# Optimization experiments

Hardware: AMD Instinct MI355X
Metric: run time of the kernel (lower is better)

The kernel has to match this reference:

```python
import jax, jax.numpy as jnp
import numpy as np

D_MODEL = 256
NUM_HEADS = 4
D_K = D_MODEL // NUM_HEADS
SCALE = float(np.sqrt(D_K))


def setup_inputs() -> dict:
    key = jax.random.key(0)
    ks = jax.random.split(key, 11)
    B, S, D = 8, 2048, D_MODEL
    inp = {
        "query": jax.random.normal(ks[0], (B, S, D), dtype=jnp.float32),
        "key": jax.random.normal(ks[1], (B, S, D), dtype=jnp.float32),
        "value": jax.random.normal(ks[2], (B, S, D), dtype=jnp.float32),
        "W_q": jax.random.normal(ks[3], (D, D), dtype=jnp.float32) / np.sqrt(D),
        "b_q": jnp.zeros((D,), dtype=jnp.float32),
        "W_k": jax.random.normal(ks[4], (D, D), dtype=jnp.float32) / np.sqrt(D),
        "b_k": jnp.zeros((D,), dtype=jnp.float32),
        "W_v": jax.random.normal(ks[5], (D, D), dtype=jnp.float32) / np.sqrt(D),
        "b_v": jnp.zeros((D,), dtype=jnp.float32),
        "W_o": jax.random.normal(ks[6], (D, D), dtype=jnp.float32) / np.sqrt(D),
        "b_o": jnp.zeros((D,), dtype=jnp.float32),
    }
    return inp


def reference(query, key, value, W_q, b_q, W_k, b_k, W_v, b_v, W_o, b_o):
    B, Sq, D = query.shape
    Sk = key.shape[1]
    H, dk = NUM_HEADS, D_K
    # projections (torch Linear equivalent: x @ W + b with W as (in,out))
    Q = (query @ W_q + b_q).reshape(B, Sq, H, dk).transpose(0, 2, 1, 3)  # (B,H,Sq,dk)
    K = (key @ W_k + b_k).reshape(B, Sk, H, dk).transpose(0, 2, 1, 3)    # (B,H,Sk,dk)
    V = value @ W_v + b_v                                                # (B,Sk,D) shared across heads
    scores = jnp.einsum("bhqd,bhkd->bhqk", Q, K) / SCALE                 # (B,H,Sq,Sk)
    attn = jax.nn.softmax(scores, axis=-1)
    avg_attn = attn.mean(axis=1)                                         # (B,Sq,Sk)
    out = jnp.einsum("bqk,bkd->bqd", avg_attn, V)
    out = out @ W_o + b_o
    return out, avg_attn
```

## Files before the change

### kernel.cpp

```cpp
#include <hip/hip_runtime.h>
#include <stdint.h>

#define S2048 2048
#define DMODEL 256
#define NH 4
#define DK 64

typedef __bf16 bf16x8 __attribute__((ext_vector_type(8)));
typedef float f32x4 __attribute__((ext_vector_type(4)));

#define MFMA16(a, b, c) __builtin_amdgcn_mfma_f32_16x16x32_bf16((a), (b), (c), 0, 0, 0)

__device__ __forceinline__ uint16_t f2bf(float f) {
  uint32_t u = __builtin_bit_cast(uint32_t, f);
  u = (u + 0x7fff + ((u >> 16) & 1)) >> 16;
  return (uint16_t)u;
}

__device__ __forceinline__ void async16(const void* g, void* l) {
  __builtin_amdgcn_global_load_lds(
      (const __attribute__((address_space(1))) unsigned int*)g,
      (__attribute__((address_space(3))) unsigned int*)l, 16, 0, 0);
}

__device__ __forceinline__ void stage64(const char* gbase, int rstride,
                                        char* lds, int tid, int rows) {
  int iters = rows >> 5;
#pragma unroll
  for (int it = 0; it < iters; ++it) {
    int cid = (it << 8) + tid;
    int m = cid >> 3, cp = cid & 7, c = cp ^ (m & 7);
    async16(gbase + (size_t)m * rstride + (c << 4),
            lds + ((size_t)((it << 8) + (tid & ~63)) << 4));
  }
}

__device__ __forceinline__ bf16x8 frag_ld(const char* t, int rowbase, int chunk, int l15) {
  int m = rowbase + l15;
  return *(const bf16x8*)(t + (((m << 3) + (chunk ^ (m & 7))) << 4));
}

__device__ __forceinline__ bf16x8 frag_ld32(const char* t, int rowbase, int chunk, int l15) {
  int m = rowbase + l15;
  return *(const bf16x8*)(t + (((m << 2) + (chunk ^ (m & 3))) << 4));
}

__global__ __launch_bounds__(256) void cast_x(const float* __restrict__ q,
                                              const float* __restrict__ k,
                                              const float* __restrict__ v,
                                              uint16_t* __restrict__ xq,
                                              uint16_t* __restrict__ xk,
                                              uint16_t* __restrict__ xv) {
  const float* src = blockIdx.y == 0 ? q : (blockIdx.y == 1 ? k : v);
  uint16_t* dst = blockIdx.y == 0 ? xq : (blockIdx.y == 1 ? xk : xv);
  size_t i = ((size_t)blockIdx.x * 256 + threadIdx.x) * 8;
  float4 a = *(const float4*)(src + i);
  float4 b = *(const float4*)(src + i + 4);
  union { uint16_t s[8]; uint4 u; } r;
  r.s[0] = f2bf(a.x); r.s[1] = f2bf(a.y); r.s[2] = f2bf(a.z); r.s[3] = f2bf(a.w);
  r.s[4] = f2bf(b.x); r.s[5] = f2bf(b.y); r.s[6] = f2bf(b.z); r.s[7] = f2bf(b.w);
  *(uint4*)(dst + i) = r.u;
}

__global__ __launch_bounds__(256) void cast_w(const float* __restrict__ Wq,
                                              const float* __restrict__ Wk,
                                              const float* __restrict__ Wv,
                                              const float* __restrict__ Wo,
                                              uint16_t* __restrict__ Wqt,
                                              uint16_t* __restrict__ Wkt,
                                              uint16_t* __restrict__ Wvt,
                                              uint16_t* __restrict__ Wot) {
  const float* W = blockIdx.y == 0 ? Wq : blockIdx.y == 1 ? Wk : blockIdx.y == 2 ? Wv : Wo;
  uint16_t* Wt = blockIdx.y == 0 ? Wqt : blockIdx.y == 1 ? Wkt : blockIdx.y == 2 ? Wvt : Wot;
  __shared__ uint16_t t[64 * 66];
  int tile = blockIdx.x, tr = tile >> 2, tc = tile & 3;
  int tid = threadIdx.x;
#pragma unroll
  for (int i = 0; i < 16; ++i) {
    int e = i * 256 + tid, r = e >> 6, cl = e & 63;
    t[r * 66 + cl] = f2bf(W[(size_t)(tr * 64 + r) * 256 + tc * 64 + cl]);
  }
  __syncthreads();
#pragma unroll
  for (int i = 0; i < 16; ++i) {
    int e = i * 256 + tid, n = e >> 6, kk = e & 63;
    Wt[(size_t)(tc * 64 + n) * 256 + tr * 64 + kk] = t[kk * 66 + n];
  }
}

template <int OUTF32, int BIAS>
__global__ __launch_bounds__(256) void gemm_bt(const uint16_t* __restrict__ A,
                                               const uint16_t* __restrict__ Bt,
                                               const float* __restrict__ bias,
                                               void* __restrict__ Cv, int K, int ldc) {
  __shared__ char lds[32768];
  char* At = lds;
  char* Btl = lds + 16384;
  int tid = threadIdx.x, lane = tid & 63, wid = tid >> 6;
  int l15 = lane & 15, q = lane >> 4;
  int mt = blockIdx.x, nt = blockIdx.y;
  int wm = (wid >> 1) * 64, wn = (wid & 1) * 64;
  f32x4 acc[4][4] = {};
  const char* Ag = (const char*)(A + (size_t)(mt * 128) * K);
  const char* Bg = (const char*)(Bt + (size_t)(nt * 128) * K);
  int nk = K >> 6;
  for (int kt = 0; kt < nk; ++kt) {
    stage64(Ag + kt * 128, K * 2, At, tid, 128);
    stage64(Bg + kt * 128, K * 2, Btl, tid, 128);
    __syncthreads();
#pragma unroll
    for (int ks = 0; ks < 2; ++ks) {
      bf16x8 a[4], b[4];
#pragma unroll
      for (int i = 0; i < 4; ++i) a[i] = frag_ld(At, wm + i * 16, ks * 4 + q, l15);
#pragma unroll
      for (int j = 0; j < 4; ++j) b[j] = frag_ld(Btl, wn + j * 16, ks * 4 + q, l15);
#pragma unroll
      for (int i = 0; i < 4; ++i)
#pragma unroll
        for (int j = 0; j < 4; ++j) acc[i][j] = MFMA16(a[i], b[j], acc[i][j]);
    }
    __syncthreads();
  }
#pragma unroll
  for (int i = 0; i < 4; ++i) {
    int r0 = mt * 128 + wm + i * 16 + q * 4;
#pragma unroll
    for (int j = 0; j < 4; ++j) {
      int c = nt * 128 + wn + j * 16 + l15;
#pragma unroll
      for (int e = 0; e < 4; ++e) {
        float v = acc[i][j][e];
        if (BIAS == 1) v += bias[c];
        if (BIAS == 2) v += bias[r0 + e];
        size_t off = (size_t)(r0 + e) * ldc + c;
        if (OUTF32) ((float*)Cv)[off] = v;
        else ((uint16_t*)Cv)[off] = f2bf(v);
      }
    }
  }
}

__global__ __launch_bounds__(256) void attn_lsum(const uint16_t* __restrict__ Qb,
                                                 const uint16_t* __restrict__ Kb,
                                                 float* __restrict__ linv4) {
  __shared__ char lds[32768];
  char* Qt = lds;
  char* Kt = lds + 16384;
  int tid = threadIdx.x, lane = tid & 63, wid = tid >> 6;
  int l15 = lane & 15, q = lane >> 4;
  int b = blockIdx.z, h = blockIdx.y, qt = blockIdx.x;
  const char* Qg = (const char*)(Qb + ((size_t)b * S2048 + qt * 128) * DMODEL + h * DK);
  const char* Kg = (const char*)(Kb + ((size_t)b * S2048) * DMODEL + h * DK);
  stage64(Qg, DMODEL * 2, Qt, tid, 128);
  float ps[2][4] = {};
  for (int kt = 0; kt < 16; ++kt) {
    stage64(Kg + (size_t)kt * 128 * (DMODEL * 2), DMODEL * 2, Kt, tid, 128);
    __syncthreads();
#pragma unroll
    for (int i = 0; i < 2; ++i) {
      bf16x8 a0 = frag_ld(Qt, wid * 32 + i * 16, q, l15);
      bf16x8 a1 = frag_ld(Qt, wid * 32 + i * 16, 4 + q, l15);
#pragma unroll
      for (int j = 0; j < 8; ++j) {
        f32x4 s = {0.f, 0.f, 0.f, 0.f};
        s = MFMA16(a0, frag_ld(Kt, j * 16, q, l15), s);
        s = MFMA16(a1, frag_ld(Kt, j * 16, 4 + q, l15), s);
#pragma unroll
        for (int e = 0; e < 4; ++e) ps[i][e] += __expf(s[e] * 0.125f);
      }
    }
    __syncthreads();
  }
#pragma unroll
  for (int i = 0; i < 2; ++i)
#pragma unroll
    for (int e = 0; e < 4; ++e) {
      float v = ps[i][e];
      v += __shfl_xor(v, 1); v += __shfl_xor(v, 2);
      v += __shfl_xor(v, 4); v += __shfl_xor(v, 8);
      if (l15 == 0) {
        int row = qt * 128 + wid * 32 + i * 16 + q * 4 + e;
        linv4[((size_t)(b * NH + h)) * S2048 + row] = 0.25f / v;
      }
    }
}

__global__ __launch_bounds__(256) void attn_fused(const uint16_t* __restrict__ Qb,
                                                  const uint16_t* __restrict__ Kb,
                                                  const uint16_t* __restrict__ VbT,
                                                  const float* __restrict__ linv4,
                                                  float* __restrict__ attn,
                                                  uint16_t* __restrict__ out1) {
  __shared__ __align__(16) char lds[51200];
  char* Kt = lds;
  char* Vt = lds + 16384;
  char* Pt = lds + 49152;
  int tid = threadIdx.x, lane = tid & 63, wid = tid >> 6;
  int l15 = lane & 15, hi = lane >> 4;
  int b = blockIdx.x & 7, qt = blockIdx.x >> 3;
  int qbase = qt * 32;
  int wq = wid & 1, wk = wid >> 1;
  int qg = wid & 1, dg = wid >> 1;
  const char* Qg = (const char*)(Qb + ((size_t)b * S2048 + qbase) * DMODEL);
  const char* Kg = (const char*)(Kb + (size_t)b * S2048 * DMODEL);
  const char* Vgb = (const char*)(VbT + (size_t)b * S2048);
#pragma unroll
  for (int h = 0; h < NH; ++h)
    stage64(Qg + h * 128, DMODEL * 2, Kt + h * 4096, tid, 32);
  float li[NH][4];
#pragma unroll
  for (int h = 0; h < NH; ++h)
#pragma unroll
    for (int e = 0; e < 4; ++e)
      li[h][e] = linv4[((size_t)(b * NH + h)) * S2048 + qbase + wq * 16 + hi * 4 + e];
  __syncthreads();
  bf16x8 qf[NH][2];
#pragma unroll
  for (int h = 0; h < NH; ++h)
#pragma unroll
    for (int ks = 0; ks < 2; ++ks)
      qf[h][ks] = frag_ld(Kt + h * 4096, wq * 16, ks * 4 + hi, l15);
  __syncthreads();
#pragma unroll
  for (int h = 0; h < NH; ++h)
    stage64(Kg + h * 128, DMODEL * 2, Kt + h * 4096, tid, 32);
  stage64(Vgb, 32768, Vt, tid, 256);
  __syncthreads();
  f32x4 acc[8] = {};
  size_t arow0 = (size_t)b * S2048 + qbase + wq * 16 + hi * 4;
#pragma unroll 2
  for (int kt = 0; kt < 64; ++kt) {
    float Pav[4] = {0.f, 0.f, 0.f, 0.f};
#pragma unroll
    for (int h = 0; h < NH; ++h) {
      f32x4 s = {0.f, 0.f, 0.f, 0.f};
      s = MFMA16(qf[h][0], frag_ld(Kt + h * 4096, wk * 16, hi, l15), s);
      s = MFMA16(qf[h][1], frag_ld(Kt + h * 4096, wk * 16, 4 + hi, l15), s);
#pragma unroll
      for (int e = 0; e < 4; ++e) Pav[e] += __expf(s[e] * 0.125f) * li[h][e];
    }
#pragma unroll
    for (int e = 0; e < 4; ++e) {
      int m = wq * 16 + hi * 4 + e, kk = wk * 16 + l15;
      *(uint16_t*)(Pt + (((m << 2) + ((kk >> 3) ^ (m & 3))) << 4) + ((kk & 7) << 1)) =
          f2bf(Pav[e]);
    }
    __syncthreads();
    {
      int kc = kt * 32 + wk * 16 + l15;
#pragma unroll
      for (int e = 0; e < 4; ++e) attn[(arow0 + e) * S2048 + kc] = Pav[e];
    }
    if (kt + 1 < 64) {
#pragma unroll
      for (int h = 0; h < NH; ++h)
        stage64(Kg + (size_t)(kt + 1) * 32 * (DMODEL * 2) + h * 128, DMODEL * 2,
                Kt + h * 4096, tid, 32);
    }
    {
      int ks = kt & 1;
      bf16x8 pa = frag_ld32(Pt, qg * 16, hi, l15);
#pragma unroll
      for (int j = 0; j < 8; ++j) {
        bf16x8 vb = frag_ld(Vt, dg * 128 + j * 16, ks * 4 + hi, l15);
        acc[j] = MFMA16(pa, vb, acc[j]);
      }
    }
    __syncthreads();
    if ((kt & 1) && kt + 1 < 64)
      stage64(Vgb + (size_t)((kt + 1) >> 1) * 128, 32768, Vt, tid, 256);
  }
#pragma unroll
  for (int j = 0; j < 8; ++j) {
    size_t r0 = (size_t)b * S2048 + qbase + qg * 16 + hi * 4;
    int c = dg * 128 + j * 16 + l15;
#pragma unroll
    for (int e = 0; e < 4; ++e) out1[(r0 + e) * DMODEL + c] = f2bf(acc[j][e]);
  }
}

extern "C" void kernel_launch(void* const* d_in, const int* in_sizes, int n_in,
                              void* d_out, int out_size, void* d_ws, size_t ws_size,
                              hipStream_t stream) {
  const float* query = (const float*)d_in[0];
  const float* key_i = (const float*)d_in[1];
  const float* value = (const float*)d_in[2];
  const float* W_q = (const float*)d_in[3];
  const float* b_q = (const float*)d_in[4];
  const float* W_k = (const float*)d_in[5];
  const float* b_k = (const float*)d_in[6];
  const float* W_v = (const float*)d_in[7];
  const float* b_v = (const float*)d_in[8];
  const float* W_o = (const float*)d_in[9];
  const float* b_o = (const float*)d_in[10];

  char* ws = (char*)d_ws;
  const size_t SZX = 16384ull * 256 * 2;
  uint16_t* Xq = (uint16_t*)(ws + 0 * SZX);
  uint16_t* Xk = (uint16_t*)(ws + 1 * SZX);
  uint16_t* Xv = (uint16_t*)(ws + 2 * SZX);
  uint16_t* Qb = (uint16_t*)(ws + 3 * SZX);
  uint16_t* Kb = (uint16_t*)(ws + 4 * SZX);
  uint16_t* VbT = (uint16_t*)(ws + 5 * SZX);
  uint16_t* out1b = (uint16_t*)(ws + 6 * SZX);
  uint16_t* Wqt = (uint16_t*)(ws + 7 * SZX);
  uint16_t* Wkt = (uint16_t*)(ws + 7 * SZX + 131072);
  uint16_t* Wvt = (uint16_t*)(ws + 7 * SZX + 2 * 131072);
  uint16_t* Wot = (uint16_t*)(ws + 7 * SZX + 3 * 131072);
  float* linv4 = (float*)(ws + 7 * SZX + 4 * 131072);

  float* out = (float*)d_out;
  float* attn = out + 16384ull * 256;

  cast_x<<<dim3(2048, 3), 256, 0, stream>>>(query, key_i, value, Xq, Xk, Xv);
  cast_w<<<dim3(16, 4), 256, 0, stream>>>(W_q, W_k, W_v, W_o, Wqt, Wkt, Wvt, Wot);
  gemm_bt<0, 1><<<dim3(128, 2), 256, 0, stream>>>(Xq, Wqt, b_q, Qb, 256, 256);
  gemm_bt<0, 1><<<dim3(128, 2), 256, 0, stream>>>(Xk, Wkt, b_k, Kb, 256, 256);
  gemm_bt<0, 2><<<dim3(2, 128), 256, 0, stream>>>(Wvt, Xv, b_v, VbT, 256, 16384);
  attn_lsum<<<dim3(16, 4, 8), 256, 0, stream>>>(Qb, Kb, linv4);
  attn_fused<<<dim3(512), 256, 0, stream>>>(Qb, Kb, VbT, linv4, attn, out1b);
  gemm_bt<1, 1><<<dim3(128, 2), 256, 0, stream>>>(out1b, Wot, b_o, out, 256, 256);
}
```

Measured before the change: 343.4 us.

## Restructure attention kernels: 512-thread fused tile, direct V loads, double-buffered lsum

Folds the 1/sqrt(dk) scale into the Q projection epilogue so the attention kernels drop a multiply before each exp. attn_lsum now hoists Q fragments into registers and double-buffers K tiles in LDS so the next tile loads while the current one computes. attn_fused moves to 512 threads with 64-key tiles, halving loop iterations and barriers, and reads V fragments straight from global memory into registers rather than staging V through LDS. This frees LDS and may improve occupancy, but adds per-lane global V loads and doubles register pressure per block, and rounding the scaled Q to bf16 slightly changes numerics.

```diff
diff --git a/kernel.cpp b/kernel.cpp
--- a/kernel.cpp
+++ b/kernel.cpp
@@ -35,14 +35,21 @@
   }
 }
 
+__device__ __forceinline__ void stage64b(const char* gbase, int rstride,
+                                         char* lds, int tid, int rows) {
+  int iters = rows >> 6;
+#pragma unroll
+  for (int it = 0; it < iters; ++it) {
+    int cid = (it << 9) + tid;
+    int m = cid >> 3, cp = cid & 7, c = cp ^ (m & 7);
+    async16(gbase + (size_t)m * rstride + (c << 4),
+            lds + ((size_t)((it << 9) + (tid & ~63)) << 4));
+  }
+}
+
 __device__ __forceinline__ bf16x8 frag_ld(const char* t, int rowbase, int chunk, int l15) {
   int m = rowbase + l15;
   return *(const bf16x8*)(t + (((m << 3) + (chunk ^ (m & 7))) << 4));
-}
-
-__device__ __forceinline__ bf16x8 frag_ld32(const char* t, int rowbase, int chunk, int l15) {
-  int m = rowbase + l15;
-  return *(const bf16x8*)(t + (((m << 2) + (chunk ^ (m & 3))) << 4));
 }
 
 __global__ __launch_bounds__(256) void cast_x(const float* __restrict__ q,
@@ -92,7 +99,8 @@
 __global__ __launch_bounds__(256) void gemm_bt(const uint16_t* __restrict__ A,
                                                const uint16_t* __restrict__ Bt,
                                                const float* __restrict__ bias,
-                                               void* __restrict__ Cv, int K, int ldc) {
+                                               void* __restrict__ Cv, int K, int ldc,
+                                               float scale) {
   __shared__ char lds[32768];
   char* At = lds;
   char* Btl = lds + 16384;
@@ -133,6 +141,7 @@
         float v = acc[i][j][e];
         if (BIAS == 1) v += bias[c];
         if (BIAS == 2) v += bias[r0 + e];
+        v *= scale;
         size_t off = (size_t)(r0 + e) * ldc + c;
         if (OUTF32) ((float*)Cv)[off] = v;
         else ((uint16_t*)Cv)[off] = f2bf(v);
@@ -144,30 +153,42 @@
 __global__ __launch_bounds__(256) void attn_lsum(const uint16_t* __restrict__ Qb,
                                                  const uint16_t* __restrict__ Kb,
                                                  float* __restrict__ linv4) {
-  __shared__ char lds[32768];
+  __shared__ char lds[49152];
   char* Qt = lds;
-  char* Kt = lds + 16384;
+  char* Kt0 = lds + 16384;
+  char* Kt1 = lds + 32768;
   int tid = threadIdx.x, lane = tid & 63, wid = tid >> 6;
   int l15 = lane & 15, q = lane >> 4;
   int b = blockIdx.z, h = blockIdx.y, qt = blockIdx.x;
   const char* Qg = (const char*)(Qb + ((size_t)b * S2048 + qt * 128) * DMODEL + h * DK);
   const char* Kg = (const char*)(Kb + ((size_t)b * S2048) * DMODEL + h * DK);
   stage64(Qg, DMODEL * 2, Qt, tid, 128);
+  stage64(Kg, DMODEL * 2, Kt0, tid, 128);
+  __syncthreads();
+  bf16x8 qf[2][2];
+#pragma unroll
+  for (int i = 0; i < 2; ++i)
+#pragma unroll
+    for (int ks = 0; ks < 2; ++ks)
+      qf[i][ks] = frag_ld(Qt, wid * 32 + i * 16, ks * 4 + q, l15);
   float ps[2][4] = {};
+#pragma unroll 1
   for (int kt = 0; kt < 16; ++kt) {
-    stage64(Kg + (size_t)kt * 128 * (DMODEL * 2), DMODEL * 2, Kt, tid, 128);
-    __syncthreads();
-#pragma unroll
-    for (int i = 0; i < 2; ++i) {
-      bf16x8 a0 = frag_ld(Qt, wid * 32 + i * 16, q, l15);
-      bf16x8 a1 = frag_ld(Qt, wid * 32 + i * 16, 4 + q, l15);
-#pragma unroll
-      for (int j = 0; j < 8; ++j) {
+    const char* Kc = (kt & 1) ? Kt1 : Kt0;
+    if (kt + 1 < 16)
+      stage64(Kg + (size_t)(kt + 1) * 128 * (DMODEL * 2), DMODEL * 2,
+              (kt & 1) ? Kt0 : Kt1, tid, 128);
+#pragma unroll
+    for (int j = 0; j < 8; ++j) {
+      bf16x8 k0 = frag_ld(Kc, j * 16, q, l15);
+      bf16x8 k1 = frag_ld(Kc, j * 16, 4 + q, l15);
+#pragma unroll
+      for (int i = 0; i < 2; ++i) {
         f32x4 s = {0.f, 0.f, 0.f, 0.f};
-        s = MFMA16(a0, frag_ld(Kt, j * 16, q, l15), s);
-        s = MFMA16(a1, frag_ld(Kt, j * 16, 4 + q, l15), s);
-#pragma unroll
-        for (int e = 0; e < 4; ++e) ps[i][e] += __expf(s[e] * 0.125f);
+        s = MFMA16(qf[i][0], k0, s);
+        s = MFMA16(qf[i][1], k1, s);
+#pragma unroll
+        for (int e = 0; e < 4; ++e) ps[i][e] += __expf(s[e]);
       }
     }
     __syncthreads();
@@ -186,16 +207,15 @@
     }
 }
 
-__global__ __launch_bounds__(256) void attn_fused(const uint16_t* __restrict__ Qb,
+__global__ __launch_bounds__(512) void attn_fused(const uint16_t* __restrict__ Qb,
                                                   const uint16_t* __restrict__ Kb,
                                                   const uint16_t* __restrict__ VbT,
                                                   const float* __restrict__ linv4,
                                                   float* __restrict__ attn,
                                                   uint16_t* __restrict__ out1) {
-  __shared__ __align__(16) char lds[51200];
+  __shared__ __align__(16) char lds[36864];
   char* Kt = lds;
-  char* Vt = lds + 16384;
-  char* Pt = lds + 49152;
+  char* Pt = lds + 32768;
   int tid = threadIdx.x, lane = tid & 63, wid = tid >> 6;
   int l15 = lane & 15, hi = lane >> 4;
   int b = blockIdx.x & 7, qt = blockIdx.x >> 3;
@@ -204,10 +224,17 @@
   int qg = wid & 1, dg = wid >> 1;
   const char* Qg = (const char*)(Qb + ((size_t)b * S2048 + qbase) * DMODEL);
   const char* Kg = (const char*)(Kb + (size_t)b * S2048 * DMODEL);
-  const char* Vgb = (const char*)(VbT + (size_t)b * S2048);
-#pragma unroll
-  for (int h = 0; h < NH; ++h)
-    stage64(Qg + h * 128, DMODEL * 2, Kt + h * 4096, tid, 32);
+  const uint16_t* Vbase =
+      VbT + (size_t)(dg * 64 + l15) * 16384 + (size_t)b * S2048 + hi * 8;
+#pragma unroll
+  for (int it = 0; it < 2; ++it) {
+    int cid = (it << 9) + tid;
+    int h = cid >> 8, r = (cid >> 3) & 31;
+    int cp = cid & 7, c = cp ^ (r & 7);
+    int g = (it << 9) + (tid & ~63);
+    async16(Qg + (size_t)r * 512 + h * 128 + (c << 4),
+            Kt + ((g & 255) << 4) + ((g >> 8) << 13));
+  }
   float li[NH][4];
 #pragma unroll
   for (int h = 0; h < NH; ++h)
@@ -220,61 +247,62 @@
   for (int h = 0; h < NH; ++h)
 #pragma unroll
     for (int ks = 0; ks < 2; ++ks)
-      qf[h][ks] = frag_ld(Kt + h * 4096, wq * 16, ks * 4 + hi, l15);
+      qf[h][ks] = frag_ld(Kt + h * 8192, wq * 16, ks * 4 + hi, l15);
   __syncthreads();
 #pragma unroll
   for (int h = 0; h < NH; ++h)
-    stage64(Kg + h * 128, DMODEL * 2, Kt + h * 4096, tid, 32);
-  stage64(Vgb, 32768, Vt, tid, 256);
-  __syncthreads();
-  f32x4 acc[8] = {};
+    stage64b(Kg + (h << 7), DMODEL * 2, Kt + h * 8192, tid, 64);
+  __syncthreads();
+  f32x4 acc[4] = {};
   size_t arow0 = (size_t)b * S2048 + qbase + wq * 16 + hi * 4;
-#pragma unroll 2
-  for (int kt = 0; kt < 64; ++kt) {
+#pragma unroll 1
+  for (int kt = 0; kt < 32; ++kt) {
+    bf16x8 vb[2][4];
+#pragma unroll
+    for (int ks = 0; ks < 2; ++ks)
+#pragma unroll
+      for (int j = 0; j < 4; ++j)
+        vb[ks][j] = *(const bf16x8*)(Vbase + (size_t)j * (16 * 16384) +
+                                     kt * 64 + ks * 32);
     float Pav[4] = {0.f, 0.f, 0.f, 0.f};
 #pragma unroll
     for (int h = 0; h < NH; ++h) {
       f32x4 s = {0.f, 0.f, 0.f, 0.f};
-      s = MFMA16(qf[h][0], frag_ld(Kt + h * 4096, wk * 16, hi, l15), s);
-      s = MFMA16(qf[h][1], frag_ld(Kt + h * 4096, wk * 16, 4 + hi, l15), s);
-#pragma unroll
-      for (int e = 0; e < 4; ++e) Pav[e] += __expf(s[e] * 0.125f) * li[h][e];
+      s = MFMA16(qf[h][0], frag_ld(Kt + h * 8192, wk * 16, hi, l15), s);
+      s = MFMA16(qf[h][1], frag_ld(Kt + h * 8192, wk * 16, 4 + hi, l15), s);
+#pragma unroll
+      for (int e = 0; e < 4; ++e) Pav[e] += __expf(s[e]) * li[h][e];
     }
 #pragma unroll
     for (int e = 0; e < 4; ++e) {
       int m = wq * 16 + hi * 4 + e, kk = wk * 16 + l15;
-      *(uint16_t*)(Pt + (((m << 2) + ((kk >> 3) ^ (m & 3))) << 4) + ((kk & 7) << 1)) =
+      *(uint16_t*)(Pt + (((m << 3) + ((kk >> 3) ^ (m & 7))) << 4) + ((kk & 7) << 1)) =
           f2bf(Pav[e]);
     }
     __syncthreads();
+    if (kt + 1 < 32) {
+#pragma unroll
+      for (int h = 0; h < NH; ++h)
+        stage64b(Kg + (size_t)(kt + 1) * 64 * (DMODEL * 2) + (h << 7), DMODEL * 2,
+                 Kt + h * 8192, tid, 64);
+    }
     {
-      int kc = kt * 32 + wk * 16 + l15;
+      int kc = kt * 64 + wk * 16 + l15;
 #pragma unroll
       for (int e = 0; e < 4; ++e) attn[(arow0 + e) * S2048 + kc] = Pav[e];
     }
-    if (kt + 1 < 64) {
-#pragma unroll
-      for (int h = 0; h < NH; ++h)
-        stage64(Kg + (size_t)(kt + 1) * 32 * (DMODEL * 2) + h * 128, DMODEL * 2,
-                Kt + h * 4096, tid, 32);
-    }
-    {
-      int ks = kt & 1;
-      bf16x8 pa = frag_ld32(Pt, qg * 16, hi, l15);
-#pragma unroll
-      for (int j = 0; j < 8; ++j) {
-        bf16x8 vb = frag_ld(Vt, dg * 128 + j * 16, ks * 4 + hi, l15);
-        acc[j] = MFMA16(pa, vb, acc[j]);
-      }
-    }
-    __syncthreads();
-    if ((kt & 1) && kt + 1 < 64)
-      stage64(Vgb + (size_t)((kt + 1) >> 1) * 128, 32768, Vt, tid, 256);
-  }
-#pragma unroll
-  for (int j = 0; j < 8; ++j) {
+#pragma unroll
+    for (int ks = 0; ks < 2; ++ks) {
+      bf16x8 pa = frag_ld(Pt, qg * 16, ks * 4 + hi, l15);
+#pragma unroll
+      for (int j = 0; j < 4; ++j) acc[j] = MFMA16(pa, vb[ks][j], acc[j]);
+    }
+    __syncthreads();
+  }
+#pragma unroll
+  for (int j = 0; j < 4; ++j) {
     size_t r0 = (size_t)b * S2048 + qbase + qg * 16 + hi * 4;
-    int c = dg * 128 + j * 16 + l15;
+    int c = dg * 64 + j * 16 + l15;
 #pragma unroll
     for (int e = 0; e < 4; ++e) out1[(r0 + e) * DMODEL + c] = f2bf(acc[j][e]);
   }
@@ -315,10 +343,10 @@
 
   cast_x<<<dim3(2048, 3), 256, 0, stream>>>(query, key_i, value, Xq, Xk, Xv);
   cast_w<<<dim3(16, 4), 256, 0, stream>>>(W_q, W_k, W_v, W_o, Wqt, Wkt, Wvt, Wot);
-  gemm_bt<0, 1><<<dim3(128, 2), 256, 0, stream>>>(Xq, Wqt, b_q, Qb, 256, 256);
-  gemm_bt<0, 1><<<dim3(128, 2), 256, 0, stream>>>(Xk, Wkt, b_k, Kb, 256, 256);
-  gemm_bt<0, 2><<<dim3(2, 128), 256, 0, stream>>>(Wvt, Xv, b_v, VbT, 256, 16384);
+  gemm_bt<0, 1><<<dim3(128, 2), 256, 0, stream>>>(Xq, Wqt, b_q, Qb, 256, 256, 0.125f);
+  gemm_bt<0, 1><<<dim3(128, 2), 256, 0, stream>>>(Xk, Wkt, b_k, Kb, 256, 256, 1.0f);
+  gemm_bt<0, 2><<<dim3(2, 128), 256, 0, stream>>>(Wvt, Xv, b_v, VbT, 256, 16384, 1.0f);
   attn_lsum<<<dim3(16, 4, 8), 256, 0, stream>>>(Qb, Kb, linv4);
-  attn_fused<<<dim3(512), 256, 0, stream>>>(Qb, Kb, VbT, linv4, attn, out1b);
-  gemm_bt<1, 1><<<dim3(128, 2), 256, 0, stream>>>(out1b, Wot, b_o, out, 256, 256);
-}
+  attn_fused<<<dim3(512), 512, 0, stream>>>(Qb, Kb, VbT, linv4, attn, out1b);
+  gemm_bt<1, 1><<<dim3(128, 2), 256, 0, stream>>>(out1b, Wot, b_o, out, 256, 256, 1.0f);
+}
```

New measurement: 401.2 us. +16.8%, slower.
